# Kernel tuning notes

Hardware: AMD Instinct MI355X
Metric: run time of the kernel (lower is better)

Reference implementation:

```python
import jax, jax.numpy as jnp
import numpy as np

N_NODES = 100000
N_EDGES = 1000000
D = 128  # latent_dim


def setup_inputs() -> dict:
    key = jax.random.key(0)
    ks = jax.random.split(key, 8)
    z = jax.random.normal(ks[0], (N_NODES, D), dtype=jnp.float32)
    edge_index = jax.random.randint(ks[1], (2, N_EDGES), 0, N_NODES, dtype=jnp.int64)
    # MLP params: Linear(2D->D), Linear(D->D//2), Linear(D//2->1)
    def lin(k, fan_in, fan_out):
        kw, kb = jax.random.split(k)
        bound = 1.0 / np.sqrt(fan_in)
        W = jax.random.uniform(kw, (fan_in, fan_out), jnp.float32, -bound, bound)
        b = jax.random.uniform(kb, (fan_out,), jnp.float32, -bound, bound)
        return W, b
    W1, b1 = lin(ks[2], 2 * D, D)
    W2, b2 = lin(ks[3], D, D // 2)
    W3, b3 = lin(ks[4], D // 2, 1)
    return {"z": z, "edge_index": edge_index, "W1": W1, "b1": b1,
            "W2": W2, "b2": b2, "W3": W3, "b3": b3}


def reference(z, edge_index, W1, b1, W2, b2, W3, b3):
    # Gather src/dst node embeddings and concat: [E, 2D]
    h = jnp.concatenate([z[edge_index[0]], z[edge_index[1]]], axis=-1)
    h = jax.nn.relu(h @ W1 + b1)      # [E, D]
    h = jax.nn.relu(h @ W2 + b2)      # [E, D//2]
    out = h @ W3 + b3                 # [E, 1]
    return out  # sigmoid=False default
```

## Files before the change

### kernel.cpp

```cpp
#include <hip/hip_runtime.h>
#include <hip/hip_bf16.h>
#include <string.h>

#define NE 1000000
#define NN 100000
#define NWT 31250
#define NGT2 3125

typedef __attribute__((ext_vector_type(8))) short bf16x8;
typedef __attribute__((ext_vector_type(4))) float f32x4;

__device__ __forceinline__ unsigned short f2bf(float f) {
  unsigned u = __builtin_bit_cast(unsigned, f);
  u += 0x7fffu + ((u >> 16) & 1u);
  return (unsigned short)(u >> 16);
}
__device__ __forceinline__ unsigned pk2(float a, float b) {
  __hip_bfloat162 h = __float22bfloat162_rn(make_float2(a, b));
  unsigned r;
  memcpy(&r, &h, 4);
  return r;
}
__device__ __forceinline__ float lo2f(unsigned u) {
  return __builtin_bit_cast(float, u << 16);
}
__device__ __forceinline__ float hi2f(unsigned u) {
  return __builtin_bit_cast(float, u & 0xffff0000u);
}

__global__ void prep(const float* __restrict__ W1, const float* __restrict__ W2,
                     unsigned short* __restrict__ afw, unsigned short* __restrict__ fw2) {
  int tid = blockIdx.x * 256 + threadIdx.x;
  if (tid < 32768) {
    int j = tid & 7, l = (tid >> 3) & 63, kb = (tid >> 9) & 3, mt = tid >> 11;
    int k = kb * 32 + (l >> 4) * 8 + j;
    int n = mt * 16 + (l & 15);
    float v = (n < 128) ? W1[k * 128 + n] : W1[(128 + k) * 128 + (n - 128)];
    afw[tid] = f2bf(v);
  } else if (tid < 40960) {
    int t = tid - 32768;
    int j = t & 7, l = (t >> 3) & 63, kb = (t >> 9) & 3, nt = t >> 11;
    fw2[t] = f2bf(W2[(kb * 32 + (l >> 4) * 8 + j) * 64 + nt * 16 + (l & 15)]);
  }
}

__global__ __launch_bounds__(256, 2) void node_gemm(
    const float* __restrict__ z, const unsigned short* __restrict__ afw,
    const float* __restrict__ b1, unsigned short* __restrict__ h1ab) {
  __shared__ __align__(16) bf16x8 sfw[4096];
  {
    const int t = threadIdx.x;
#pragma unroll
    for (int it = 0; it < 16; it++)
      sfw[it * 256 + t] = ((const bf16x8*)afw)[it * 256 + t];
  }
  __syncthreads();

  const int l = threadIdx.x & 63, w = threadIdx.x >> 6;
  const int wt = blockIdx.x * 4 + w;
  if (wt >= NGT2) return;
  const int c = l & 15, g = l >> 4;
  const int n0 = wt * 32;

  float4 zl[2][4][2];
#pragma unroll
  for (int grp = 0; grp < 2; grp++)
#pragma unroll
    for (int kb = 0; kb < 4; kb++) {
      const float* zp = z + (n0 + grp * 16 + c) * 128 + kb * 32 + g * 8;
      zl[grp][kb][0] = *(const float4*)zp;
      zl[grp][kb][1] = *(const float4*)(zp + 4);
    }

  f32x4 acc[2][16] = {};
#pragma unroll
  for (int kb = 0; kb < 4; kb++) {
    bf16x8 bfrag[2];
#pragma unroll
    for (int grp = 0; grp < 2; grp++) {
      float4 a = zl[grp][kb][0], b = zl[grp][kb][1];
      uint4 u = {pk2(a.x, a.y), pk2(a.z, a.w), pk2(b.x, b.y), pk2(b.z, b.w)};
      bfrag[grp] = __builtin_bit_cast(bf16x8, u);
    }
#pragma unroll
    for (int mt = 0; mt < 16; mt++) {
      bf16x8 af = sfw[(mt * 4 + kb) * 64 + l];
      acc[0][mt] = __builtin_amdgcn_mfma_f32_16x16x32_bf16(af, bfrag[0], acc[0][mt], 0, 0, 0);
      acc[1][mt] = __builtin_amdgcn_mfma_f32_16x16x32_bf16(af, bfrag[1], acc[1][mt], 0, 0, 0);
    }
  }

#pragma unroll
  for (int grp = 0; grp < 2; grp++)
#pragma unroll
    for (int mt = 0; mt < 16; mt++) {
      const int f0 = mt * 16 + g * 4;
      float v0 = acc[grp][mt][0], v1 = acc[grp][mt][1];
      float v2 = acc[grp][mt][2], v3 = acc[grp][mt][3];
      if (mt < 8) {
        float4 bb = *(const float4*)(b1 + f0);
        v0 += bb.x; v1 += bb.y; v2 += bb.z; v3 += bb.w;
      }
      uint2 pk = {pk2(v0, v1), pk2(v2, v3)};
      *(uint2*)(h1ab + (n0 + grp * 16 + c) * 256 + f0) = pk;
    }
}

__global__ __launch_bounds__(256, 4) void mlp_edge(
    const unsigned short* __restrict__ h1ab, const int* __restrict__ edge,
    const unsigned short* __restrict__ fw2,
    const float* __restrict__ b2, const float* __restrict__ W3,
    const float* __restrict__ b3, float* __restrict__ out) {
  __shared__ __align__(16) unsigned short sfw2[8192];
  {
    const int t = threadIdx.x;
#pragma unroll
    for (int it = 0; it < 4; it++)
      ((bf16x8*)sfw2)[it * 256 + t] = ((const bf16x8*)fw2)[it * 256 + t];
  }
  __syncthreads();

  const int l = threadIdx.x & 63, w = threadIdx.x >> 6;
  const int wt = blockIdx.x * 4 + w;
  if (wt >= NWT) return;
  const int c = l & 15, g = l >> 4;
  const int eBase = wt * 32;

  const char* hb = (const char*)h1ab;
  const unsigned kbase = (unsigned)g * 16u;

  uint4 sv[2][4], dv[2][4];
#pragma unroll
  for (int mt = 0; mt < 2; mt++) {
    int e = eBase + mt * 16 + c;
    unsigned so = (unsigned)edge[e] * 512u + kbase;
    unsigned dofs = (unsigned)edge[NE + e] * 512u + 256u + kbase;
#pragma unroll
    for (int kb = 0; kb < 4; kb++) {
      sv[mt][kb] = *(const uint4*)(hb + so + kb * 64u);
      dv[mt][kb] = *(const uint4*)(hb + dofs + kb * 64u);
    }
  }

  f32x4 acc2[2][4] = {};
#pragma unroll
  for (int kb = 0; kb < 4; kb++) {
    bf16x8 a2[2];
#pragma unroll
    for (int mt = 0; mt < 2; mt++) {
      uint4 s = sv[mt][kb], d = dv[mt][kb];
      uint4 r;
      r.x = pk2(fmaxf(lo2f(s.x) + lo2f(d.x), 0.f), fmaxf(hi2f(s.x) + hi2f(d.x), 0.f));
      r.y = pk2(fmaxf(lo2f(s.y) + lo2f(d.y), 0.f), fmaxf(hi2f(s.y) + hi2f(d.y), 0.f));
      r.z = pk2(fmaxf(lo2f(s.z) + lo2f(d.z), 0.f), fmaxf(hi2f(s.z) + hi2f(d.z), 0.f));
      r.w = pk2(fmaxf(lo2f(s.w) + lo2f(d.w), 0.f), fmaxf(hi2f(s.w) + hi2f(d.w), 0.f));
      a2[mt] = __builtin_bit_cast(bf16x8, r);
    }
#pragma unroll
    for (int nt = 0; nt < 4; nt++) {
      bf16x8 bf = ((const bf16x8*)sfw2)[(nt * 4 + kb) * 64 + l];
#pragma unroll
      for (int mt = 0; mt < 2; mt++)
        acc2[mt][nt] = __builtin_amdgcn_mfma_f32_16x16x32_bf16(a2[mt], bf, acc2[mt][nt], 0, 0, 0);
    }
  }

  float w3v[4], b2v[4];
#pragma unroll
  for (int nt = 0; nt < 4; nt++) {
    w3v[nt] = W3[nt * 16 + c];
    b2v[nt] = b2[nt * 16 + c];
  }
  const float bias3 = b3[0];
#pragma unroll
  for (int mt = 0; mt < 2; mt++) {
#pragma unroll
    for (int i = 0; i < 4; i++) {
      float t = 0.f;
#pragma unroll
      for (int nt = 0; nt < 4; nt++)
        t += fmaxf(acc2[mt][nt][i] + b2v[nt], 0.f) * w3v[nt];
      t += __shfl_xor(t, 1);
      t += __shfl_xor(t, 2);
      t += __shfl_xor(t, 4);
      t += __shfl_xor(t, 8);
      if (c == 0) out[eBase + mt * 16 + g * 4 + i] = t + bias3;
    }
  }
}

extern "C" void kernel_launch(void* const* d_in, const int* in_sizes, int n_in,
                              void* d_out, int out_size, void* d_ws, size_t ws_size,
                              hipStream_t stream) {
  const float* z  = (const float*)d_in[0];
  const int* edge = (const int*)d_in[1];
  const float* W1 = (const float*)d_in[2];
  const float* b1 = (const float*)d_in[3];
  const float* W2 = (const float*)d_in[4];
  const float* b2 = (const float*)d_in[5];
  const float* W3 = (const float*)d_in[6];
  const float* b3 = (const float*)d_in[7];
  float* out = (float*)d_out;

  unsigned short* afw  = (unsigned short*)d_ws;
  unsigned short* fw2  = afw + 32768;
  unsigned short* h1ab = fw2 + 8192;

  prep<<<160, 256, 0, stream>>>(W1, W2, afw, fw2);
  node_gemm<<<(NGT2 + 3) / 4, 256, 0, stream>>>(z, afw, b1, h1ab);
  mlp_edge<<<(NWT + 3) / 4, 256, 0, stream>>>(h1ab, edge, fw2, b2, W3, b3, out);
}
```

Measured before the change: 204.8 us.

## Make edge kernel persistent with k-block prefetch; drop LDS from node GEMM

The edge MLP kernel becomes a grid-stride persistent kernel with 977 blocks, each wave handling up to 8 tiles of 32 edges. This spreads the LDS weight load over more work. Inside each tile the gathers are software-pipelined: the next k-block's src/dst rows are loaded while the current block runs its MFMAs, which lowers register pressure compared with loading everything up front. The node GEMM now handles 16 nodes per wave instead of 32 and reads the W1 fragments straight from global memory instead of staging them in LDS, with a higher occupancy bound. The risk is more global and L2 traffic for the weights and less latency hiding in the gather, since fewer loads are in flight at once.

```diff
diff --git a/kernel.cpp b/kernel.cpp
--- a/kernel.cpp
+++ b/kernel.cpp
@@ -5,7 +5,8 @@
 #define NE 1000000
 #define NN 100000
 #define NWT 31250
-#define NGT2 3125
+#define NGT 6250
+#define EWB 977
 
 typedef __attribute__((ext_vector_type(8))) short bf16x8;
 typedef __attribute__((ext_vector_type(4))) float f32x4;
@@ -44,66 +45,47 @@
   }
 }
 
-__global__ __launch_bounds__(256, 2) void node_gemm(
+__global__ __launch_bounds__(256, 4) void node_gemm(
     const float* __restrict__ z, const unsigned short* __restrict__ afw,
     const float* __restrict__ b1, unsigned short* __restrict__ h1ab) {
-  __shared__ __align__(16) bf16x8 sfw[4096];
-  {
-    const int t = threadIdx.x;
-#pragma unroll
-    for (int it = 0; it < 16; it++)
-      sfw[it * 256 + t] = ((const bf16x8*)afw)[it * 256 + t];
-  }
-  __syncthreads();
-
   const int l = threadIdx.x & 63, w = threadIdx.x >> 6;
   const int wt = blockIdx.x * 4 + w;
-  if (wt >= NGT2) return;
+  if (wt >= NGT) return;
   const int c = l & 15, g = l >> 4;
-  const int n0 = wt * 32;
-
-  float4 zl[2][4][2];
-#pragma unroll
-  for (int grp = 0; grp < 2; grp++)
-#pragma unroll
-    for (int kb = 0; kb < 4; kb++) {
-      const float* zp = z + (n0 + grp * 16 + c) * 128 + kb * 32 + g * 8;
-      zl[grp][kb][0] = *(const float4*)zp;
-      zl[grp][kb][1] = *(const float4*)(zp + 4);
-    }
-
-  f32x4 acc[2][16] = {};
+  const int n0 = wt * 16;
+
+  const float* zrow = z + (n0 + c) * 128;
+  float4 zl[4][2];
 #pragma unroll
   for (int kb = 0; kb < 4; kb++) {
-    bf16x8 bfrag[2];
-#pragma unroll
-    for (int grp = 0; grp < 2; grp++) {
-      float4 a = zl[grp][kb][0], b = zl[grp][kb][1];
-      uint4 u = {pk2(a.x, a.y), pk2(a.z, a.w), pk2(b.x, b.y), pk2(b.z, b.w)};
-      bfrag[grp] = __builtin_bit_cast(bf16x8, u);
-    }
+    zl[kb][0] = *(const float4*)(zrow + kb * 32 + g * 8);
+    zl[kb][1] = *(const float4*)(zrow + kb * 32 + g * 8 + 4);
+  }
+
+  f32x4 acc[16] = {};
+#pragma unroll
+  for (int kb = 0; kb < 4; kb++) {
+    float4 a = zl[kb][0], b = zl[kb][1];
+    uint4 u = {pk2(a.x, a.y), pk2(a.z, a.w), pk2(b.x, b.y), pk2(b.z, b.w)};
+    bf16x8 bfrag = __builtin_bit_cast(bf16x8, u);
 #pragma unroll
     for (int mt = 0; mt < 16; mt++) {
-      bf16x8 af = sfw[(mt * 4 + kb) * 64 + l];
-      acc[0][mt] = __builtin_amdgcn_mfma_f32_16x16x32_bf16(af, bfrag[0], acc[0][mt], 0, 0, 0);
-      acc[1][mt] = __builtin_amdgcn_mfma_f32_16x16x32_bf16(af, bfrag[1], acc[1][mt], 0, 0, 0);
-    }
-  }
-
-#pragma unroll
-  for (int grp = 0; grp < 2; grp++)
-#pragma unroll
-    for (int mt = 0; mt < 16; mt++) {
-      const int f0 = mt * 16 + g * 4;
-      float v0 = acc[grp][mt][0], v1 = acc[grp][mt][1];
-      float v2 = acc[grp][mt][2], v3 = acc[grp][mt][3];
-      if (mt < 8) {
-        float4 bb = *(const float4*)(b1 + f0);
-        v0 += bb.x; v1 += bb.y; v2 += bb.z; v3 += bb.w;
-      }
-      uint2 pk = {pk2(v0, v1), pk2(v2, v3)};
-      *(uint2*)(h1ab + (n0 + grp * 16 + c) * 256 + f0) = pk;
-    }
+      bf16x8 af = *(const bf16x8*)(afw + ((mt * 4 + kb) * 64 + l) * 8);
+      acc[mt] = __builtin_amdgcn_mfma_f32_16x16x32_bf16(af, bfrag, acc[mt], 0, 0, 0);
+    }
+  }
+
+#pragma unroll
+  for (int mt = 0; mt < 16; mt++) {
+    const int f0 = mt * 16 + g * 4;
+    float v0 = acc[mt][0], v1 = acc[mt][1], v2 = acc[mt][2], v3 = acc[mt][3];
+    if (mt < 8) {
+      float4 bb = *(const float4*)(b1 + f0);
+      v0 += bb.x; v1 += bb.y; v2 += bb.z; v3 += bb.w;
+    }
+    uint2 pk = {pk2(v0, v1), pk2(v2, v3)};
+    *(uint2*)(h1ab + (n0 + c) * 256 + f0) = pk;
+  }
 }
 
 __global__ __launch_bounds__(256, 4) void mlp_edge(
@@ -115,55 +97,16 @@
   {
     const int t = threadIdx.x;
 #pragma unroll
-    for (int it = 0; it < 4; it++)
-      ((bf16x8*)sfw2)[it * 256 + t] = ((const bf16x8*)fw2)[it * 256 + t];
+    for (int st = 0; st < 4; st++)
+      ((bf16x8*)sfw2)[st * 256 + t] = ((const bf16x8*)fw2)[st * 256 + t];
   }
   __syncthreads();
 
   const int l = threadIdx.x & 63, w = threadIdx.x >> 6;
-  const int wt = blockIdx.x * 4 + w;
-  if (wt >= NWT) return;
+  const int wslot = blockIdx.x * 4 + w;
   const int c = l & 15, g = l >> 4;
-  const int eBase = wt * 32;
-
+  const unsigned kbase = (unsigned)g * 16u;
   const char* hb = (const char*)h1ab;
-  const unsigned kbase = (unsigned)g * 16u;
-
-  uint4 sv[2][4], dv[2][4];
-#pragma unroll
-  for (int mt = 0; mt < 2; mt++) {
-    int e = eBase + mt * 16 + c;
-    unsigned so = (unsigned)edge[e] * 512u + kbase;
-    unsigned dofs = (unsigned)edge[NE + e] * 512u + 256u + kbase;
-#pragma unroll
-    for (int kb = 0; kb < 4; kb++) {
-      sv[mt][kb] = *(const uint4*)(hb + so + kb * 64u);
-      dv[mt][kb] = *(const uint4*)(hb + dofs + kb * 64u);
-    }
-  }
-
-  f32x4 acc2[2][4] = {};
-#pragma unroll
-  for (int kb = 0; kb < 4; kb++) {
-    bf16x8 a2[2];
-#pragma unroll
-    for (int mt = 0; mt < 2; mt++) {
-      uint4 s = sv[mt][kb], d = dv[mt][kb];
-      uint4 r;
-      r.x = pk2(fmaxf(lo2f(s.x) + lo2f(d.x), 0.f), fmaxf(hi2f(s.x) + hi2f(d.x), 0.f));
-      r.y = pk2(fmaxf(lo2f(s.y) + lo2f(d.y), 0.f), fmaxf(hi2f(s.y) + hi2f(d.y), 0.f));
-      r.z = pk2(fmaxf(lo2f(s.z) + lo2f(d.z), 0.f), fmaxf(hi2f(s.z) + hi2f(d.z), 0.f));
-      r.w = pk2(fmaxf(lo2f(s.w) + lo2f(d.w), 0.f), fmaxf(hi2f(s.w) + hi2f(d.w), 0.f));
-      a2[mt] = __builtin_bit_cast(bf16x8, r);
-    }
-#pragma unroll
-    for (int nt = 0; nt < 4; nt++) {
-      bf16x8 bf = ((const bf16x8*)sfw2)[(nt * 4 + kb) * 64 + l];
-#pragma unroll
-      for (int mt = 0; mt < 2; mt++)
-        acc2[mt][nt] = __builtin_amdgcn_mfma_f32_16x16x32_bf16(a2[mt], bf, acc2[mt][nt], 0, 0, 0);
-    }
-  }
 
   float w3v[4], b2v[4];
 #pragma unroll
@@ -172,19 +115,70 @@
     b2v[nt] = b2[nt * 16 + c];
   }
   const float bias3 = b3[0];
-#pragma unroll
-  for (int mt = 0; mt < 2; mt++) {
-#pragma unroll
-    for (int i = 0; i < 4; i++) {
-      float t = 0.f;
-#pragma unroll
-      for (int nt = 0; nt < 4; nt++)
-        t += fmaxf(acc2[mt][nt][i] + b2v[nt], 0.f) * w3v[nt];
-      t += __shfl_xor(t, 1);
-      t += __shfl_xor(t, 2);
-      t += __shfl_xor(t, 4);
-      t += __shfl_xor(t, 8);
-      if (c == 0) out[eBase + mt * 16 + g * 4 + i] = t + bias3;
+
+  for (int it = 0; it < 8; it++) {
+    const int wt = wslot + it * (EWB * 4);
+    if (wt >= NWT) break;
+    const int eBase = wt * 32;
+    const int e0 = eBase + c;
+    const unsigned so0 = (unsigned)edge[e0] * 512u + kbase;
+    const unsigned so1 = (unsigned)edge[e0 + 16] * 512u + kbase;
+    const unsigned do0 = (unsigned)edge[NE + e0] * 512u + 256u + kbase;
+    const unsigned do1 = (unsigned)edge[NE + e0 + 16] * 512u + 256u + kbase;
+
+    uint4 svc[2], dvc[2], svn[2], dvn[2];
+    svc[0] = *(const uint4*)(hb + so0);
+    svc[1] = *(const uint4*)(hb + so1);
+    dvc[0] = *(const uint4*)(hb + do0);
+    dvc[1] = *(const uint4*)(hb + do1);
+
+    f32x4 acc2[2][4] = {};
+#pragma unroll
+    for (int kb = 0; kb < 4; kb++) {
+      if (kb < 3) {
+        const unsigned o = (unsigned)(kb + 1) * 64u;
+        svn[0] = *(const uint4*)(hb + so0 + o);
+        svn[1] = *(const uint4*)(hb + so1 + o);
+        dvn[0] = *(const uint4*)(hb + do0 + o);
+        dvn[1] = *(const uint4*)(hb + do1 + o);
+      }
+      bf16x8 a2[2];
+#pragma unroll
+      for (int mt = 0; mt < 2; mt++) {
+        uint4 s = svc[mt], d = dvc[mt];
+        uint4 r;
+        r.x = pk2(fmaxf(lo2f(s.x) + lo2f(d.x), 0.f), fmaxf(hi2f(s.x) + hi2f(d.x), 0.f));
+        r.y = pk2(fmaxf(lo2f(s.y) + lo2f(d.y), 0.f), fmaxf(hi2f(s.y) + hi2f(d.y), 0.f));
+        r.z = pk2(fmaxf(lo2f(s.z) + lo2f(d.z), 0.f), fmaxf(hi2f(s.z) + hi2f(d.z), 0.f));
+        r.w = pk2(fmaxf(lo2f(s.w) + lo2f(d.w), 0.f), fmaxf(hi2f(s.w) + hi2f(d.w), 0.f));
+        a2[mt] = __builtin_bit_cast(bf16x8, r);
+      }
+#pragma unroll
+      for (int nt = 0; nt < 4; nt++) {
+        bf16x8 bf = ((const bf16x8*)sfw2)[(nt * 4 + kb) * 64 + l];
+        acc2[0][nt] = __builtin_amdgcn_mfma_f32_16x16x32_bf16(a2[0], bf, acc2[0][nt], 0, 0, 0);
+        acc2[1][nt] = __builtin_amdgcn_mfma_f32_16x16x32_bf16(a2[1], bf, acc2[1][nt], 0, 0, 0);
+      }
+      if (kb < 3) {
+#pragma unroll
+        for (int mt = 0; mt < 2; mt++) { svc[mt] = svn[mt]; dvc[mt] = dvn[mt]; }
+      }
+    }
+
+#pragma unroll
+    for (int mt = 0; mt < 2; mt++) {
+#pragma unroll
+      for (int i = 0; i < 4; i++) {
+        float t = 0.f;
+#pragma unroll
+        for (int nt = 0; nt < 4; nt++)
+          t += fmaxf(acc2[mt][nt][i] + b2v[nt], 0.f) * w3v[nt];
+        t += __shfl_xor(t, 1);
+        t += __shfl_xor(t, 2);
+        t += __shfl_xor(t, 4);
+        t += __shfl_xor(t, 8);
+        if (c == 0) out[eBase + mt * 16 + g * 4 + i] = t + bias3;
+      }
     }
   }
 }
@@ -207,6 +201,6 @@
   unsigned short* h1ab = fw2 + 8192;
 
   prep<<<160, 256, 0, stream>>>(W1, W2, afw, fw2);
-  node_gemm<<<(NGT2 + 3) / 4, 256, 0, stream>>>(z, afw, b1, h1ab);
-  mlp_edge<<<(NWT + 3) / 4, 256, 0, stream>>>(h1ab, edge, fw2, b2, W3, b3, out);
-}
+  node_gemm<<<(NGT + 3) / 4, 256, 0, stream>>>(z, afw, b1, h1ab);
+  mlp_edge<<<EWB, 256, 0, stream>>>(h1ab, edge, fw2, b2, W3, b3, out);
+}
```

After: 213.2 us. 4.1% more time.
